# Kernel tuning notes

Measured on AMD Instinct MI355X. Metric: run time of the kernel, lower is better.

The kernel has to match this reference:

```python
import jax, jax.numpy as jnp
import numpy as np

B, D, X, Y = 16, 64, 48, 48
DI = 128            # interactions_dim
DIN = D + 2         # depth_dim + 2 coord channels (qst_dim = 0)


def setup_inputs() -> dict:
    key = jax.random.key(0)
    k1, k2, k3, k4 = jax.random.split(key, 4)
    x = jax.random.normal(k1, (B, D, X, Y), dtype=jnp.float32)
    s = 1.0 / np.sqrt(DIN)  # torch Linear default init range
    Wq = jax.random.uniform(k2, (DI, DIN), jnp.float32, -s, s)
    Wk = jax.random.uniform(k3, (DI, DIN), jnp.float32, -s, s)
    Wv = jax.random.uniform(k4, (DI, DIN), jnp.float32, -s, s)
    return {"x": x, "Wq": Wq, "Wk": Wk, "Wv": Wv}


def _add_xy(x):
    # addXYfeatures: append normalized grid coords, flatten spatial dims
    b, d, sx, sy = x.shape
    fx = -1.0 + (jnp.arange(sx, dtype=x.dtype) + 0.5) * (2.0 / sx)
    fy = -1.0 + (jnp.arange(sy, dtype=x.dtype) + 0.5) * (2.0 / sy)
    fxy = jnp.broadcast_to(fx[None, None, :, None], (b, 1, sx, sy))
    fyx = jnp.broadcast_to(fy[None, None, None, :], (b, 1, sx, sy))
    aug = jnp.concatenate([x, fxy, fyx], axis=1)  # [B, D+2, X, Y]
    return aug.reshape(b, d + 2, sx * sy)          # [B, D+2, N]


def reference(x, Wq, Wk, Wv):
    aug = _add_xy(x)                               # [B, Din, N]
    e = jnp.transpose(aug, (0, 2, 1))              # [B, N, Din] entities
    q = jnp.einsum('bnd,ed->bne', e, Wq)           # [B, N, DI]
    k = jnp.einsum('bnd,ed->bne', e, Wk)
    v = jnp.einsum('bnd,ed->bne', e, Wv)
    scale = 1.0 / jnp.sqrt(jnp.asarray(DI, dtype=x.dtype))
    scores = jnp.einsum('bqe,bke->bqk', q, k) * scale  # [B, Nq, Nk]
    # torch: F.softmax(..., dim=0) on per-batch [Nq, Nk] -> axis=1 here (over queries)
    att = jax.nn.softmax(scores, axis=1)
    out = jnp.einsum('bqk,bkd->bqd', att, v)       # [B, N, DI]
    return out
```

## Files before the change

kernel.cpp:

```cpp
#include <hip/hip_runtime.h>
#include <cstdint>

#define B_    16
#define D_    64
#define N_    2304
#define DI_   128
#define S2_   0.12751875732488788f
#define NB_   ((size_t)B_ * N_ * DI_)
#define KTSZ_ 4096
#define VTSZ_ 5120
#define NKT_  72
#define NKH_  18
#define OF4_  1179648

typedef __attribute__((ext_vector_type(8)))  short short8v;
typedef __attribute__((ext_vector_type(16))) float f32x16;

#if defined(__has_builtin)
#if __has_builtin(__builtin_amdgcn_exp2f)
#define EXP2(x) __builtin_amdgcn_exp2f(x)
#else
#define EXP2(x) exp2f(x)
#endif
#else
#define EXP2(x) exp2f(x)
#endif

__device__ __forceinline__ unsigned short f2bf(float f) {
    unsigned u = __builtin_bit_cast(unsigned, f);
    u = (u + 0x7FFFu + ((u >> 16) & 1u)) >> 16;
    return (unsigned short)u;
}
__device__ __forceinline__ float bf2f(unsigned short h) {
    unsigned u = ((unsigned)h) << 16;
    return __builtin_bit_cast(float, u);
}
__device__ __forceinline__ unsigned cvtpk_bf16(float lo, float hi) {
    unsigned r;
    asm volatile("v_cvt_pk_bf16_f32 %0, %1, %2" : "=v"(r) : "v"(lo), "v"(hi));
    return r;
}
__device__ __forceinline__ void plswap(unsigned &a, unsigned &b) {
    asm volatile("v_permlane32_swap_b32 %0, %1" : "+v"(a), "+v"(b));
}

__device__ __forceinline__ void stage_k(const unsigned short* g,
                                        unsigned short* l_, int w, int ln) {
    #pragma unroll
    for (int i = 0; i < 2; ++i)
        __builtin_amdgcn_global_load_lds(
            (const __attribute__((address_space(1))) void*)(g + i * 2048 + w * 512 + ln * 8),
            (__attribute__((address_space(3))) void*)(l_ + i * 2048 + w * 512), 16, 0, 0);
}
__device__ __forceinline__ void stage_v(const unsigned short* g,
                                        unsigned short* l_, int w, int ln, int t) {
    #pragma unroll
    for (int i = 0; i < 2; ++i)
        __builtin_amdgcn_global_load_lds(
            (const __attribute__((address_space(1))) void*)(g + i * 2048 + w * 512 + ln * 8),
            (__attribute__((address_space(3))) void*)(l_ + i * 2048 + w * 512), 16, 0, 0);
    if (t < 128)
        __builtin_amdgcn_global_load_lds(
            (const __attribute__((address_space(1))) void*)(g + 4096 + w * 512 + ln * 8),
            (__attribute__((address_space(3))) void*)(l_ + 4096 + w * 512), 16, 0, 0);
}

__global__ __launch_bounds__(256) void prep_kernel(
    const float* __restrict__ Wq, const float* __restrict__ Wk,
    const float* __restrict__ Wv, unsigned short* __restrict__ W3p,
    float* __restrict__ Zg)
{
    const int t = threadIdx.x;
    if (blockIdx.x == 0) {
        for (int r = t; r < 384; r += 256) {
            const float* src = (r < 128) ? (Wq + r * 66)
                             : (r < 256) ? (Wk + (r - 128) * 66) : (Wv + (r - 256) * 66);
            for (int c = 0; c < 66; ++c) W3p[r * 88 + c] = f2bf(src[c]);
            for (int c = 66; c < 88; ++c) W3p[r * 88 + c] = 0;
        }
    } else {
        Zg[(blockIdx.x - 1) * 256 + t] = 0.0f;
    }
}

__global__ __launch_bounds__(256) void qkv_kernel(
    const float* __restrict__ x, const unsigned short* __restrict__ W3p,
    unsigned short* __restrict__ Qb, unsigned short* __restrict__ Ksw,
    unsigned short* __restrict__ Vn)
{
    __shared__ unsigned short Es[128 * 88];
    const int t = threadIdx.x;
    const int b = blockIdx.x / 18, nt = blockIdx.x - b * 18;
    const int n0 = nt * 128;

    {
        const int d = t & 63, q4 = t >> 6;
        const float* xp = x + ((size_t)b * D_ + d) * N_ + n0 + q4 * 32;
        float xv[32];
        #pragma unroll
        for (int i = 0; i < 8; ++i) *(float4*)(xv + 4 * i) = *(const float4*)(xp + 4 * i);
        #pragma unroll
        for (int i = 0; i < 32; ++i) Es[(q4 * 32 + i) * 88 + d] = f2bf(xv[i]);
    }
    if (t < 128) {
        int n = n0 + t;
        int ix = n / 48, iy = n - ix * 48;
        Es[t * 88 + 64] = f2bf(-1.0f + ((float)ix + 0.5f) * (2.0f / 48.0f));
        Es[t * 88 + 65] = f2bf(-1.0f + ((float)iy + 0.5f) * (2.0f / 48.0f));
        #pragma unroll
        for (int m = 0; m < 11; ++m) *(unsigned*)&Es[t * 88 + 66 + 2 * m] = 0;
    }
    __syncthreads();

    const int l = t & 63, w = t >> 6;
    const int m32 = l & 31, H = l >> 5;
    const int colbase = w * 96;
    #pragma unroll
    for (int nf = 0; nf < 4; ++nf) {
        f32x16 acc[3];
        #pragma unroll
        for (int of = 0; of < 3; ++of)
            #pragma unroll
            for (int i = 0; i < 16; ++i) acc[of][i] = 0.0f;
        #pragma unroll
        for (int kc = 0; kc < 5; ++kc) {
            short8v a = *(const short8v*)&Es[(nf * 32 + m32) * 88 + kc * 16 + H * 8];
            #pragma unroll
            for (int of = 0; of < 3; ++of) {
                short8v bf = *(const short8v*)&W3p[(colbase + of * 32 + m32) * 88 + kc * 16 + H * 8];
                acc[of] = __builtin_amdgcn_mfma_f32_32x32x16_bf16(a, bf, acc[of], 0, 0, 0);
            }
        }
        #pragma unroll
        for (int of = 0; of < 3; ++of) {
            const int col0 = colbase + of * 32;
            const int mi = col0 >> 7, e0 = col0 & 127;
            const int e = e0 + m32;
            if (mi == 0) {
                #pragma unroll
                for (int r = 0; r < 16; ++r) {
                    int n = n0 + nf * 32 + (r & 3) + 8 * (r >> 2) + 4 * H;
                    Qb[((size_t)b * N_ + n) * DI_ + e] = f2bf(acc[of][r] * S2_);
                }
            } else if (mi == 1) {
                const size_t tbase = ((size_t)b * NKT_ + nt * 4 + nf) * KTSZ_;
                const int cx = e >> 3, ei = e & 7;
                #pragma unroll
                for (int r = 0; r < 16; ++r) {
                    int rr = (r & 3) + 8 * (r >> 2) + 4 * H;
                    Ksw[tbase + rr * 128 + ((cx ^ (rr & 15)) * 8) + ei] = f2bf(acc[of][r]);
                }
            } else {
                #pragma unroll
                for (int r = 0; r < 16; ++r) {
                    int n = n0 + nf * 32 + (r & 3) + 8 * (r >> 2) + 4 * H;
                    Vn[((size_t)b * N_ + n) * DI_ + e] = f2bf(acc[of][r]);
                }
            }
        }
    }
}

__global__ __launch_bounds__(256, 3) void zsum_kernel(
    const unsigned short* __restrict__ Qb, const unsigned short* __restrict__ Ksw,
    float* __restrict__ Zg)
{
    __shared__ unsigned short Ks0[KTSZ_], Ks1[KTSZ_];
    __shared__ float Zacc[576];
    const int t = threadIdx.x;
    const int blk = blockIdx.x;
    const int b = 2 * (blk & 7) + ((blk >> 3) & 1);
    const int rest = blk >> 4;
    const int qt = rest % 9, kh = rest / 9;
    const int q0 = qt * 256;
    const int l = t & 63, w = t >> 6;
    const int m32 = l & 31, H = l >> 5;

    for (int i = t; i < 576; i += 256) Zacc[i] = 0.0f;

    short8v qreg[2][8];
    {
        const unsigned short* qp = Qb + ((size_t)b * N_ + q0 + w * 64 + m32) * DI_ + H * 8;
        #pragma unroll
        for (int qf = 0; qf < 2; ++qf)
            #pragma unroll
            for (int ec = 0; ec < 8; ++ec)
                qreg[qf][ec] = *(const short8v*)(qp + (size_t)qf * 32 * DI_ + ec * 16);
    }
    int ka[8];
    #pragma unroll
    for (int ec = 0; ec < 8; ++ec)
        ka[ec] = m32 * 128 + (((ec * 2 + H) ^ (m32 & 15)) * 8);

    const unsigned short* kswb = Ksw + ((size_t)b * NKT_ + kh * NKH_) * KTSZ_;
    stage_k(kswb, Ks0, w, l);
    asm volatile("s_waitcnt vmcnt(0)" ::: "memory");
    __syncthreads();

#define ZSTEP(KB, KTC)                                                         \
    {                                                                          \
        f32x16 s0, s1;                                                         \
        _Pragma("unroll") for (int i = 0; i < 16; ++i) { s0[i] = 0.f; s1[i] = 0.f; } \
        __builtin_amdgcn_s_setprio(1);                                         \
        _Pragma("unroll") for (int ec = 0; ec < 8; ++ec) {                     \
            short8v bk = *(const short8v*)&(KB)[ka[ec]];                       \
            s0 = __builtin_amdgcn_mfma_f32_32x32x16_bf16(qreg[0][ec], bk, s0, 0, 0, 0); \
            s1 = __builtin_amdgcn_mfma_f32_32x32x16_bf16(qreg[1][ec], bk, s1, 0, 0, 0); \
        }                                                                      \
        __builtin_amdgcn_s_setprio(0);                                         \
        float zl = 0.0f;                                                       \
        _Pragma("unroll") for (int r = 0; r < 16; ++r)                         \
            zl += EXP2(s0[r]) + EXP2(s1[r]);                                   \
        atomicAdd(&Zacc[(KTC) * 32 + m32], zl);                                \
        asm volatile("s_waitcnt vmcnt(0)" ::: "memory");                       \
        __syncthreads();                                                       \
    }

    for (int g = 0; g < 9; ++g) {
        const int kt = 2 * g;
        stage_k(kswb + (size_t)(kt + 1) * KTSZ_, Ks1, w, l);
        ZSTEP(Ks0, kt);
        if (kt + 2 < NKH_) stage_k(kswb + (size_t)(kt + 2) * KTSZ_, Ks0, w, l);
        ZSTEP(Ks1, kt + 1);
    }
#undef ZSTEP

    for (int i = t; i < 576; i += 256)
        atomicAdd(&Zg[(size_t)b * N_ + kh * 576 + i], Zacc[i]);
}

__global__ __launch_bounds__(256) void repackV_kernel(
    const unsigned short* __restrict__ Vn, const float* __restrict__ Zg,
    unsigned short* __restrict__ Vsw)
{
    __shared__ unsigned short Vstg[32 * 132];
    __shared__ float zinv[32];
    const int blk = blockIdx.x;
    const int b = blk / NKT_, kt = blk - b * NKT_;
    const int t = threadIdx.x;
    const int k0 = kt * 32;
    {
        const int k = t >> 3, c = (t & 7) * 16;
        const unsigned short* src = Vn + ((size_t)b * N_ + k0 + k) * DI_ + c;
        *(int4*)&Vstg[k * 132 + c]     = *(const int4*)(src);
        *(int4*)&Vstg[k * 132 + c + 8] = *(const int4*)(src + 8);
    }
    if (t < 32) zinv[t] = 1.0f / Zg[(size_t)b * N_ + k0 + t];
    __syncthreads();
    unsigned short* dstt = Vsw + ((size_t)b * NKT_ + kt) * VTSZ_;
    const int d = t & 127, part = t >> 7;
    #pragma unroll
    for (int g = 0; g < 4; ++g) {
        unsigned short sv[4];
        #pragma unroll
        for (int j = 0; j < 4; ++j) {
            int k = part * 16 + g * 4 + j;
            sv[j] = f2bf(bf2f(Vstg[k * 132 + d]) * zinv[k]);
        }
        *(int2*)(dstt + d * 40 + part * 16 + g * 4) = *(const int2*)sv;
    }
}

__global__ __launch_bounds__(256, 3) void attn_kernel(
    const unsigned short* __restrict__ Qb, const unsigned short* __restrict__ Ksw,
    const unsigned short* __restrict__ Vsw,
    float* __restrict__ O0, float* __restrict__ Op)
{
    __shared__ unsigned short Ks0[KTSZ_], Ks1[KTSZ_];
    __shared__ unsigned short Vs0[VTSZ_], Vs1[VTSZ_];
    const int t = threadIdx.x;
    const int blk = blockIdx.x;
    const int b = 2 * (blk & 7) + ((blk >> 3) & 1);
    const int rest = blk >> 4;
    const int qt = rest % 18, kh = rest / 18;
    const int q0 = qt * 128;
    const int l = t & 63, w = t >> 6;
    const int m32 = l & 31, H = l >> 5;

    short8v qreg[8];
    {
        const unsigned short* qp = Qb + ((size_t)b * N_ + q0 + w * 32 + m32) * DI_ + H * 8;
        #pragma unroll
        for (int ec = 0; ec < 8; ++ec) qreg[ec] = *(const short8v*)(qp + ec * 16);
    }
    f32x16 oacc[4];
    #pragma unroll
    for (int df = 0; df < 4; ++df)
        #pragma unroll
        for (int i = 0; i < 16; ++i) oacc[df][i] = 0.0f;

    int ka[8];
    #pragma unroll
    for (int ec = 0; ec < 8; ++ec)
        ka[ec] = m32 * 128 + (((ec * 2 + H) ^ (m32 & 15)) * 8);
    const int vb0 = m32 * 40 + H * 8;

    const unsigned short* kswb = Ksw + ((size_t)b * NKT_ + kh * NKH_) * KTSZ_;
    const unsigned short* vswb = Vsw + ((size_t)b * NKT_ + kh * NKH_) * VTSZ_;
    stage_k(kswb, Ks0, w, l);
    stage_v(vswb, Vs0, w, l, t);
    asm volatile("s_waitcnt vmcnt(0)" ::: "memory");
    __syncthreads();

#define PSTEP(KB, VB)                                                          \
    {                                                                          \
        f32x16 sacc;                                                           \
        _Pragma("unroll") for (int i = 0; i < 16; ++i) sacc[i] = 0.f;          \
        __builtin_amdgcn_s_setprio(1);                                         \
        _Pragma("unroll") for (int ec = 0; ec < 8; ++ec) {                     \
            short8v ak = *(const short8v*)&(KB)[ka[ec]];                       \
            sacc = __builtin_amdgcn_mfma_f32_32x32x16_bf16(ak, qreg[ec], sacc, 0, 0, 0); \
        }                                                                      \
        __builtin_amdgcn_s_setprio(0);                                         \
        unsigned c0[4], c1[4];                                                 \
        _Pragma("unroll") for (int m = 0; m < 4; ++m) {                        \
            float e0 = EXP2(sacc[4 * m]),     e1 = EXP2(sacc[4 * m + 1]);      \
            float e2 = EXP2(sacc[4 * m + 2]), e3 = EXP2(sacc[4 * m + 3]);      \
            c0[m] = cvtpk_bf16(e0, e1);                                        \
            c1[m] = cvtpk_bf16(e2, e3);                                        \
        }                                                                      \
        short8v pB[2];                                                         \
        _Pragma("unroll") for (int kq = 0; kq < 2; ++kq) {                     \
            unsigned d0 = c0[2 * kq], d2 = c0[2 * kq + 1]; plswap(d0, d2);     \
            unsigned d1 = c1[2 * kq], d3 = c1[2 * kq + 1]; plswap(d1, d3);     \
            int4 t4; t4.x = (int)d0; t4.y = (int)d1; t4.z = (int)d2; t4.w = (int)d3; \
            pB[kq] = __builtin_bit_cast(short8v, t4);                          \
        }                                                                      \
        __builtin_amdgcn_s_setprio(1);                                         \
        _Pragma("unroll") for (int df = 0; df < 4; ++df) {                     \
            _Pragma("unroll") for (int kq = 0; kq < 2; ++kq) {                 \
                short8v av = *(const short8v*)&(VB)[vb0 + df * 1280 + kq * 16]; \
                oacc[df] = __builtin_amdgcn_mfma_f32_32x32x16_bf16(av, pB[kq], oacc[df], 0, 0, 0); \
            }                                                                  \
        }                                                                      \
        __builtin_amdgcn_s_setprio(0);                                         \
        asm volatile("s_waitcnt vmcnt(0)" ::: "memory");                       \
        __syncthreads();                                                       \
    }

    for (int kt = 0; kt < NKH_; kt += 2) {
        stage_k(kswb + (size_t)(kt + 1) * KTSZ_, Ks1, w, l);
        stage_v(vswb + (size_t)(kt + 1) * VTSZ_, Vs1, w, l, t);
        PSTEP(Ks0, Vs0);
        if (kt + 2 < NKH_) {
            stage_k(kswb + (size_t)(kt + 2) * KTSZ_, Ks0, w, l);
            stage_v(vswb + (size_t)(kt + 2) * VTSZ_, Vs0, w, l, t);
        }
        PSTEP(Ks1, Vs1);
    }
#undef PSTEP

    float* outp = (kh == 0 ? O0 : (Op + (size_t)(kh - 1) * NB_))
                + ((size_t)b * N_ + q0 + w * 32 + m32) * DI_;
    #pragma unroll
    for (int df = 0; df < 4; ++df)
        #pragma unroll
        for (int r = 0; r < 16; ++r) {
            int d = df * 32 + (r & 3) + 8 * (r >> 2) + 4 * H;
            outp[d] = oacc[df][r];
        }
}

__global__ __launch_bounds__(256) void reduce_kernel(
    float* __restrict__ out, const float* __restrict__ part)
{
    const size_t idx = (size_t)blockIdx.x * 256 + threadIdx.x;
    float4 p0 = ((const float4*)part)[idx];
    float4 p1 = ((const float4*)part)[idx + (size_t)OF4_];
    float4 p2 = ((const float4*)part)[idx + 2 * (size_t)OF4_];
    float4 o  = ((float4*)out)[idx];
    o.x += p0.x + p1.x + p2.x;
    o.y += p0.y + p1.y + p2.y;
    o.z += p0.z + p1.z + p2.z;
    o.w += p0.w + p1.w + p2.w;
    ((float4*)out)[idx] = o;
}

extern "C" void kernel_launch(void* const* d_in, const int* in_sizes, int n_in,
                              void* d_out, int out_size, void* d_ws, size_t ws_size,
                              hipStream_t stream)
{
    const float* x  = (const float*)d_in[0];
    const float* Wq = (const float*)d_in[1];
    const float* Wk = (const float*)d_in[2];
    const float* Wv = (const float*)d_in[3];

    unsigned short* Qb  = (unsigned short*)d_ws;
    unsigned short* Ksw = Qb  + NB_;
    unsigned short* Vsw = Ksw + NB_;
    unsigned short* W3p = Vsw + (size_t)B_ * NKT_ * VTSZ_;
    float*          Zg  = (float*)(W3p + 384 * 88);
    float*          Op  = Zg + (size_t)B_ * N_;
    unsigned short* Vn  = (unsigned short*)Op;
    float* out = (float*)d_out;

    prep_kernel   <<<145,  256, 0, stream>>>(Wq, Wk, Wv, W3p, Zg);
    qkv_kernel    <<<288,  256, 0, stream>>>(x, W3p, Qb, Ksw, Vn);
    zsum_kernel   <<<576,  256, 0, stream>>>(Qb, Ksw, Zg);
    repackV_kernel<<<1152, 256, 0, stream>>>(Vn, Zg, Vsw);
    attn_kernel   <<<1152, 256, 0, stream>>>(Qb, Ksw, Vsw, out, Op);
    reduce_kernel <<<4608, 256, 0, stream>>>(out, Op);
}
```

Measured before the change: 146.5 us.

## Stage two key tiles per sync and halve attention key-split partials

The zsum and attention kernels now load two K (and V) tiles per stage into doubled LDS buffers, so there is one wait-and-barrier per pair of tiles instead of one per tile. The attention kernel splits the keys into two halves instead of four, launching half as many blocks with two blocks per CU in the launch bounds. The reduce kernel therefore adds only one partial buffer. The aim is fewer barriers and less partial-output traffic, at the cost of larger LDS use, lower occupancy and fewer blocks to fill the GPU.

```diff
diff --git a/kernel.cpp b/kernel.cpp
--- a/kernel.cpp
+++ b/kernel.cpp
@@ -10,7 +10,6 @@
 #define KTSZ_ 4096
 #define VTSZ_ 5120
 #define NKT_  72
-#define NKH_  18
 #define OF4_  1179648
 
 typedef __attribute__((ext_vector_type(8)))  short short8v;
@@ -44,25 +43,22 @@
     asm volatile("v_permlane32_swap_b32 %0, %1" : "+v"(a), "+v"(b));
 }
 
-__device__ __forceinline__ void stage_k(const unsigned short* g,
-                                        unsigned short* l_, int w, int ln) {
-    #pragma unroll
-    for (int i = 0; i < 2; ++i)
-        __builtin_amdgcn_global_load_lds(
-            (const __attribute__((address_space(1))) void*)(g + i * 2048 + w * 512 + ln * 8),
-            (__attribute__((address_space(3))) void*)(l_ + i * 2048 + w * 512), 16, 0, 0);
-}
-__device__ __forceinline__ void stage_v(const unsigned short* g,
-                                        unsigned short* l_, int w, int ln, int t) {
-    #pragma unroll
-    for (int i = 0; i < 2; ++i)
-        __builtin_amdgcn_global_load_lds(
-            (const __attribute__((address_space(1))) void*)(g + i * 2048 + w * 512 + ln * 8),
-            (__attribute__((address_space(3))) void*)(l_ + i * 2048 + w * 512), 16, 0, 0);
-    if (t < 128)
-        __builtin_amdgcn_global_load_lds(
-            (const __attribute__((address_space(1))) void*)(g + 4096 + w * 512 + ln * 8),
-            (__attribute__((address_space(3))) void*)(l_ + 4096 + w * 512), 16, 0, 0);
+__device__ __forceinline__ void gld_lds(const unsigned short* g, unsigned short* l_) {
+    __builtin_amdgcn_global_load_lds(
+        (const __attribute__((address_space(1))) void*)g,
+        (__attribute__((address_space(3))) void*)l_, 16, 0, 0);
+}
+__device__ __forceinline__ void stage_k2(const unsigned short* g,
+                                         unsigned short* l_, int w, int ln) {
+    #pragma unroll
+    for (int i = 0; i < 4; ++i)
+        gld_lds(g + i * 2048 + w * 512 + ln * 8, l_ + i * 2048 + w * 512);
+}
+__device__ __forceinline__ void stage_v2(const unsigned short* g,
+                                         unsigned short* l_, int w, int ln) {
+    #pragma unroll
+    for (int i = 0; i < 5; ++i)
+        gld_lds(g + i * 2048 + w * 512 + ln * 8, l_ + i * 2048 + w * 512);
 }
 
 __global__ __launch_bounds__(256) void prep_kernel(
@@ -165,7 +161,7 @@
     const unsigned short* __restrict__ Qb, const unsigned short* __restrict__ Ksw,
     float* __restrict__ Zg)
 {
-    __shared__ unsigned short Ks0[KTSZ_], Ks1[KTSZ_];
+    __shared__ unsigned short Ks0[2 * KTSZ_], Ks1[2 * KTSZ_];
     __shared__ float Zacc[576];
     const int t = threadIdx.x;
     const int blk = blockIdx.x;
@@ -192,8 +188,8 @@
     for (int ec = 0; ec < 8; ++ec)
         ka[ec] = m32 * 128 + (((ec * 2 + H) ^ (m32 & 15)) * 8);
 
-    const unsigned short* kswb = Ksw + ((size_t)b * NKT_ + kh * NKH_) * KTSZ_;
-    stage_k(kswb, Ks0, w, l);
+    const unsigned short* kswb = Ksw + ((size_t)b * NKT_ + kh * 18) * KTSZ_;
+    stage_k2(kswb, Ks0, w, l);
     asm volatile("s_waitcnt vmcnt(0)" ::: "memory");
     __syncthreads();
 
@@ -212,18 +208,24 @@
         _Pragma("unroll") for (int r = 0; r < 16; ++r)                         \
             zl += EXP2(s0[r]) + EXP2(s1[r]);                                   \
         atomicAdd(&Zacc[(KTC) * 32 + m32], zl);                                \
-        asm volatile("s_waitcnt vmcnt(0)" ::: "memory");                       \
-        __syncthreads();                                                       \
-    }
-
-    for (int g = 0; g < 9; ++g) {
-        const int kt = 2 * g;
-        stage_k(kswb + (size_t)(kt + 1) * KTSZ_, Ks1, w, l);
-        ZSTEP(Ks0, kt);
-        if (kt + 2 < NKH_) stage_k(kswb + (size_t)(kt + 2) * KTSZ_, Ks0, w, l);
-        ZSTEP(Ks1, kt + 1);
-    }
+    }
+#define ZDRAIN()                                                               \
+    asm volatile("s_waitcnt vmcnt(0)" ::: "memory");                           \
+    __syncthreads();
+
+    for (int pp = 0; pp < 4; ++pp) {
+        const int P0 = 2 * pp, P1 = P0 + 1;
+        stage_k2(kswb + (size_t)(P0 + 1) * 2 * KTSZ_, Ks1, w, l);
+        ZSTEP(Ks0, 2 * P0); ZSTEP(Ks0 + KTSZ_, 2 * P0 + 1);
+        ZDRAIN();
+        stage_k2(kswb + (size_t)(P1 + 1) * 2 * KTSZ_, Ks0, w, l);
+        ZSTEP(Ks1, 2 * P1); ZSTEP(Ks1 + KTSZ_, 2 * P1 + 1);
+        ZDRAIN();
+    }
+    ZSTEP(Ks0, 16); ZSTEP(Ks0 + KTSZ_, 17);
+    __syncthreads();
 #undef ZSTEP
+#undef ZDRAIN
 
     for (int i = t; i < 576; i += 256)
         atomicAdd(&Zg[(size_t)b * N_ + kh * 576 + i], Zacc[i]);
@@ -261,13 +263,13 @@
     }
 }
 
-__global__ __launch_bounds__(256, 3) void attn_kernel(
+__global__ __launch_bounds__(256, 2) void attn_kernel(
     const unsigned short* __restrict__ Qb, const unsigned short* __restrict__ Ksw,
     const unsigned short* __restrict__ Vsw,
     float* __restrict__ O0, float* __restrict__ Op)
 {
-    __shared__ unsigned short Ks0[KTSZ_], Ks1[KTSZ_];
-    __shared__ unsigned short Vs0[VTSZ_], Vs1[VTSZ_];
+    __shared__ unsigned short Ks0[2 * KTSZ_], Ks1[2 * KTSZ_];
+    __shared__ unsigned short Vs0[2 * VTSZ_], Vs1[2 * VTSZ_];
     const int t = threadIdx.x;
     const int blk = blockIdx.x;
     const int b = 2 * (blk & 7) + ((blk >> 3) & 1);
@@ -295,10 +297,10 @@
         ka[ec] = m32 * 128 + (((ec * 2 + H) ^ (m32 & 15)) * 8);
     const int vb0 = m32 * 40 + H * 8;
 
-    const unsigned short* kswb = Ksw + ((size_t)b * NKT_ + kh * NKH_) * KTSZ_;
-    const unsigned short* vswb = Vsw + ((size_t)b * NKT_ + kh * NKH_) * VTSZ_;
-    stage_k(kswb, Ks0, w, l);
-    stage_v(vswb, Vs0, w, l, t);
+    const unsigned short* kswb = Ksw + ((size_t)b * NKT_ + kh * 36) * KTSZ_;
+    const unsigned short* vswb = Vsw + ((size_t)b * NKT_ + kh * 36) * VTSZ_;
+    stage_k2(kswb, Ks0, w, l);
+    stage_v2(vswb, Vs0, w, l);
     asm volatile("s_waitcnt vmcnt(0)" ::: "memory");
     __syncthreads();
 
@@ -334,23 +336,28 @@
             }                                                                  \
         }                                                                      \
         __builtin_amdgcn_s_setprio(0);                                         \
-        asm volatile("s_waitcnt vmcnt(0)" ::: "memory");                       \
-        __syncthreads();                                                       \
-    }
-
-    for (int kt = 0; kt < NKH_; kt += 2) {
-        stage_k(kswb + (size_t)(kt + 1) * KTSZ_, Ks1, w, l);
-        stage_v(vswb + (size_t)(kt + 1) * VTSZ_, Vs1, w, l, t);
-        PSTEP(Ks0, Vs0);
-        if (kt + 2 < NKH_) {
-            stage_k(kswb + (size_t)(kt + 2) * KTSZ_, Ks0, w, l);
-            stage_v(vswb + (size_t)(kt + 2) * VTSZ_, Vs0, w, l, t);
-        }
-        PSTEP(Ks1, Vs1);
+    }
+#define PDRAIN()                                                               \
+    asm volatile("s_waitcnt vmcnt(0)" ::: "memory");                           \
+    __syncthreads();
+
+    for (int pp = 0; pp < 9; ++pp) {
+        const int P0 = 2 * pp, P1 = P0 + 1;
+        stage_k2(kswb + (size_t)(P0 + 1) * 2 * KTSZ_, Ks1, w, l);
+        stage_v2(vswb + (size_t)(P0 + 1) * 2 * VTSZ_, Vs1, w, l);
+        PSTEP(Ks0, Vs0); PSTEP(Ks0 + KTSZ_, Vs0 + VTSZ_);
+        PDRAIN();
+        if (P1 + 1 < 18) {
+            stage_k2(kswb + (size_t)(P1 + 1) * 2 * KTSZ_, Ks0, w, l);
+            stage_v2(vswb + (size_t)(P1 + 1) * 2 * VTSZ_, Vs0, w, l);
+        }
+        PSTEP(Ks1, Vs1); PSTEP(Ks1 + KTSZ_, Vs1 + VTSZ_);
+        PDRAIN();
     }
 #undef PSTEP
-
-    float* outp = (kh == 0 ? O0 : (Op + (size_t)(kh - 1) * NB_))
+#undef PDRAIN
+
+    float* outp = (kh == 0 ? O0 : Op)
                 + ((size_t)b * N_ + q0 + w * 32 + m32) * DI_;
     #pragma unroll
     for (int df = 0; df < 4; ++df)
@@ -366,13 +373,8 @@
 {
     const size_t idx = (size_t)blockIdx.x * 256 + threadIdx.x;
     float4 p0 = ((const float4*)part)[idx];
-    float4 p1 = ((const float4*)part)[idx + (size_t)OF4_];
-    float4 p2 = ((const float4*)part)[idx + 2 * (size_t)OF4_];
     float4 o  = ((float4*)out)[idx];
-    o.x += p0.x + p1.x + p2.x;
-    o.y += p0.y + p1.y + p2.y;
-    o.z += p0.z + p1.z + p2.z;
-    o.w += p0.w + p1.w + p2.w;
+    o.x += p0.x; o.y += p0.y; o.z += p0.z; o.w += p0.w;
     ((float4*)out)[idx] = o;
 }
 
@@ -398,6 +400,6 @@
     qkv_kernel    <<<288,  256, 0, stream>>>(x, W3p, Qb, Ksw, Vn);
     zsum_kernel   <<<576,  256, 0, stream>>>(Qb, Ksw, Zg);
     repackV_kernel<<<1152, 256, 0, stream>>>(Vn, Zg, Vsw);
-    attn_kernel   <<<1152, 256, 0, stream>>>(Qb, Ksw, Vsw, out, Op);
+    attn_kernel   <<<576,  256, 0, stream>>>(Qb, Ksw, Vsw, out, Op);
     reduce_kernel <<<4608, 256, 0, stream>>>(out, Op);
 }
```

New measurement: 148.9 us. About the same (+1.6%).
